# Optimization experiments

Hardware: AMD Instinct MI355X
Metric: run time of the kernel (lower is better)

## Reference

```python
import jax, jax.numpy as jnp
import numpy as np

N, E = 100000, 1600000
IN_C, HID, OUT_C = 128, 128, 64
HOPS, L = 2, 3
EPS = 1e-5


def setup_inputs() -> dict:
    key = jax.random.key(0)
    ks = jax.random.split(key, 16)
    x = jax.random.normal(ks[0], (N, IN_C), jnp.float32)
    edge_index = jax.random.randint(ks[1], (2, E), 0, N, dtype=jnp.int32).astype(jnp.int64)
    CAT = HID * (HOPS + 1)  # 384
    def lin(k, fan_in, fan_out, nstack):
        return jax.random.normal(k, (nstack, fan_in, fan_out), jnp.float32) / np.sqrt(fan_in)
    return {
        "x": x,
        "edge_index": edge_index,
        "W0": lin(ks[2], IN_C, HID, HOPS + 1),
        "b0": jnp.zeros((HOPS + 1, HID), jnp.float32),
        "W1": lin(ks[3], CAT, HID, HOPS + 1),
        "b1": jnp.zeros((HOPS + 1, HID), jnp.float32),
        "W2": lin(ks[4], CAT, OUT_C, HOPS + 1),
        "b2": jnp.zeros((HOPS + 1, OUT_C), jnp.float32),
        "bn0_g": jnp.ones((CAT,), jnp.float32),
        "bn0_b": jnp.zeros((CAT,), jnp.float32),
        "bn1_g": jnp.ones((CAT,), jnp.float32),
        "bn1_b": jnp.zeros((CAT,), jnp.float32),
        "fpW": jax.random.normal(ks[5], (OUT_C * (HOPS + 1), OUT_C), jnp.float32) / np.sqrt(OUT_C * (HOPS + 1)),
        "fpb": jnp.zeros((OUT_C,), jnp.float32),
    }


def reference(x, edge_index, W0, b0, W1, b1, W2, b2,
              bn0_g, bn0_b, bn1_g, bn1_b, fpW, fpb):
    row, col = edge_index[0], edge_index[1]
    # gcn_norm with add_self_loops=False, unit edge weights:
    # deg = scatter_add(1, col); w_e = deg^-1/2[row] * deg^-1/2[col]
    deg = jnp.zeros((N,), x.dtype).at[col].add(1.0)
    dinv = jnp.where(deg > 0, jax.lax.rsqrt(jnp.maximum(deg, 1.0)), 0.0)
    ew = dinv[row] * dinv[col]

    def spmm(h):
        # adj_t = SparseTensor(row=col, col=row, value=ew): out[col] += ew * h[row]
        return jax.ops.segment_sum(ew[:, None] * h[row], col, num_segments=N)

    def mixhop(h, W, b):
        outs = []
        for j in range(HOPS + 1):
            hj = h @ W[j] + b[j]          # lins[j](h)
            for _ in range(j):
                hj = spmm(hj)             # A^j applied j times
            outs.append(hj)
        return jnp.concatenate(outs, axis=1)

    def bn(h, g, bb):
        # BatchNorm1d in training mode: batch stats, biased variance
        mu = h.mean(axis=0)
        var = h.var(axis=0)
        return g * (h - mu) * jax.lax.rsqrt(var + EPS) + bb

    h = jax.nn.relu(bn(mixhop(x, W0, b0), bn0_g, bn0_b))   # dropout: identity (eval)
    h = jax.nn.relu(bn(mixhop(h, W1, b1), bn1_g, bn1_b))
    h = mixhop(h, W2, b2)
    return h @ fpW + fpb
```

## Files before the change

### kernel.cpp

```cpp
#include <hip/hip_runtime.h>
#include <cstdint>
#include <cstddef>

#define IN_C 128
#define HIDc 128
#define OUTc 64

using bf8 = __attribute__((ext_vector_type(8))) __bf16;
using f4  = __attribute__((ext_vector_type(4))) float;

__device__ __forceinline__ unsigned short f2bf(float f) {
    unsigned int u = __float_as_uint(f);
    unsigned int r = (u + 0x7FFFu + ((u >> 16) & 1u)) >> 16;
    return (unsigned short)r;
}
__device__ __forceinline__ float bf2f(unsigned short h) {
    return __uint_as_float(((unsigned int)h) << 16);
}

__global__ void k_detect(const long long* ei, int n_nodes, int* flag) {
    int t = threadIdx.x;
    long long v = ei[t];
    int ok = (v >= 0 && v < (long long)n_nodes) ? 1 : 0;
    unsigned long long m = __ballot(ok);
    if (t == 0) *flag = (m == ~0ull) ? 1 : 0;
}

__global__ void k_cvt_hist(const void* ei, int twoE, int E, const int* flag,
                           int* __restrict__ out, int* __restrict__ deg, int n) {
    int i = blockIdx.x * blockDim.x + threadIdx.x;
    if (i >= twoE) return;
    int v = (*flag) ? (int)((const long long*)ei)[i] : ((const int*)ei)[i];
    out[i] = v;
    if (i >= E && (unsigned)v < (unsigned)n) atomicAdd(&deg[v], 1);
}

__global__ void k_dinv(const int* __restrict__ deg, float* __restrict__ dinv, int n) {
    int i = blockIdx.x * blockDim.x + threadIdx.x;
    if (i < n) dinv[i] = (deg[i] > 0) ? rsqrtf((float)deg[i]) : 0.0f;
}

__global__ void k_alloc(const int* __restrict__ deg, int* __restrict__ base,
                        int* __restrict__ cursor, int* __restrict__ counter, int n) {
    int i = blockIdx.x * blockDim.x + threadIdx.x;
    int lane = threadIdx.x & 63;
    int val = (i < n) ? deg[i] : 0;
    int scan = val;
    #pragma unroll
    for (int off = 1; off < 64; off <<= 1) {
        int t = __shfl_up(scan, off);
        if (lane >= off) scan += t;
    }
    int excl = scan - val;
    int total = __shfl(scan, 63);
    int wb = 0;
    if (lane == 0) wb = atomicAdd(counter, total);
    wb = __shfl(wb, 0);
    if (i < n) { base[i] = wb + excl; cursor[i] = wb + excl; }
}

__global__ void k_scatter(const int* __restrict__ eint, int E,
                          const float* __restrict__ dinv, int n,
                          int* __restrict__ cursor, int2* __restrict__ ew) {
    int e = blockIdx.x * blockDim.x + threadIdx.x;
    if (e >= E) return;
    int r = eint[e];
    int c = eint[E + e];
    if ((unsigned)r >= (unsigned)n || (unsigned)c >= (unsigned)n) return;
    int p = atomicAdd(&cursor[c], 1);
    int2 v; v.x = r; v.y = __float_as_int(dinv[r] * dinv[c]);
    ew[p] = v;
}

__global__ void k_wprep(const float* __restrict__ W, unsigned short* __restrict__ Wt,
                        int K, int N) {
    int j = blockIdx.y;
    int idx = blockIdx.x * 256 + threadIdx.x;
    if (idx >= K * N) return;
    int k = idx / N, nn = idx - k * N;
    Wt[(size_t)j * N * K + (size_t)nn * K + k] = f2bf(W[(size_t)j * K * N + idx]);
}

__global__ void k_cast4(const float* __restrict__ x, unsigned short* __restrict__ y, int n4) {
    int i = blockIdx.x * 256 + threadIdx.x;
    if (i >= n4) return;
    float4 v = ((const float4*)x)[i];
    ushort4 o;
    o.x = f2bf(v.x); o.y = f2bf(v.y); o.z = f2bf(v.z); o.w = f2bf(v.w);
    ((ushort4*)y)[i] = o;
}

template<int PW, bool AFFINE>
__global__ __launch_bounds__(512) void k_mfma3(
    const unsigned short* __restrict__ A0, const unsigned short* __restrict__ A1,
    const unsigned short* __restrict__ A2, int W, int M, int K,
    const unsigned short* __restrict__ Bt, const float* __restrict__ bias,
    const float* __restrict__ scale, const float* __restrict__ shift,
    unsigned short* __restrict__ C0, unsigned short* __restrict__ C1,
    unsigned short* __restrict__ C2)
{
    constexpr int NT = 3 * PW;
    constexpr int TN = NT / 64;
    int t = threadIdx.x;
    int wave = t >> 6, lane = t & 63;
    int m16 = lane & 15, q = lane >> 4;
    int rowHalf = wave & 1, colQ = wave >> 1;
    int row0 = blockIdx.x * 128;

    size_t aoff[4];
    #pragma unroll
    for (int tm = 0; tm < 4; tm++) {
        int r = row0 + rowHalf * 64 + tm * 16 + m16;
        if (r >= M) r = M - 1;
        aoff[tm] = (size_t)r * W;
    }
    size_t boff[TN];
    #pragma unroll
    for (int tn = 0; tn < TN; tn++)
        boff[tn] = (size_t)(colQ * 16 * TN + tn * 16 + m16) * K;

    f4 acc[4][TN];
    #pragma unroll
    for (int i = 0; i < 4; i++)
        #pragma unroll
        for (int j = 0; j < TN; j++) acc[i][j] = (f4){0.f, 0.f, 0.f, 0.f};

    for (int kk = 0; kk < K; kk += 32) {
        int pi = kk / W;
        const unsigned short* Ap = (pi == 0) ? A0 : ((pi == 1) ? A1 : A2);
        int kl = kk - pi * W;

        uint4 a4[4];
        #pragma unroll
        for (int tm = 0; tm < 4; tm++)
            a4[tm] = *(const uint4*)&Ap[aoff[tm] + kl + q * 8];

        if (AFFINE) {
            int ch0 = kk + q * 8;
            float scv[8], shv[8];
            *(float4*)&scv[0] = *(const float4*)&scale[ch0];
            *(float4*)&scv[4] = *(const float4*)&scale[ch0 + 4];
            *(float4*)&shv[0] = *(const float4*)&shift[ch0];
            *(float4*)&shv[4] = *(const float4*)&shift[ch0 + 4];
            #pragma unroll
            for (int tm = 0; tm < 4; tm++) {
                unsigned int* w32 = (unsigned int*)&a4[tm];
                #pragma unroll
                for (int h = 0; h < 4; h++) {
                    unsigned int u = w32[h];
                    float lo = fmaxf(bf2f((unsigned short)(u & 0xffff)) * scv[2*h]     + shv[2*h],     0.f);
                    float hi = fmaxf(bf2f((unsigned short)(u >> 16))    * scv[2*h + 1] + shv[2*h + 1], 0.f);
                    w32[h] = (unsigned int)f2bf(lo) | ((unsigned int)f2bf(hi) << 16);
                }
            }
        }

        bf8 bfr[TN];
        #pragma unroll
        for (int tn = 0; tn < TN; tn++)
            bfr[tn] = *(const bf8*)&Bt[boff[tn] + kk + q * 8];

        #pragma unroll
        for (int tm = 0; tm < 4; tm++) {
            bf8 af = *(const bf8*)&a4[tm];
            #pragma unroll
            for (int tn = 0; tn < TN; tn++)
                acc[tm][tn] = __builtin_amdgcn_mfma_f32_16x16x32_bf16(
                    af, bfr[tn], acc[tm][tn], 0, 0, 0);
        }
    }

    #pragma unroll
    for (int tn = 0; tn < TN; tn++) {
        int col_base = colQ * 16 * TN + tn * 16;
        int j  = col_base / PW;
        int cc = col_base - j * PW + m16;
        unsigned short* Cj = (j == 0) ? C0 : ((j == 1) ? C1 : C2);
        float bi = bias[col_base + m16];
        #pragma unroll
        for (int tm = 0; tm < 4; tm++) {
            #pragma unroll
            for (int r = 0; r < 4; r++) {
                int row = row0 + rowHalf * 64 + tm * 16 + q * 4 + r;
                if (row >= M) continue;
                Cj[(size_t)row * PW + cc] = f2bf(acc[tm][tn][r] + bi);
            }
        }
    }
}

__global__ __launch_bounds__(256) void k_mfma_fin(
    const unsigned short* __restrict__ A0, const unsigned short* __restrict__ A1,
    const unsigned short* __restrict__ A2, int W, int M, int K,
    const unsigned short* __restrict__ Bt, const float* __restrict__ bias,
    float* __restrict__ C, int ldc)
{
    constexpr int TM = 2, TN = 4;
    int t = threadIdx.x;
    int wave = t >> 6, lane = t & 63;
    int m16 = lane & 15, q = lane >> 4;
    int row0 = blockIdx.x * 128;
    int wr = wave * 32;

    size_t aoff[TM];
    #pragma unroll
    for (int tm = 0; tm < TM; tm++) {
        int r = row0 + wr + tm * 16 + m16;
        if (r >= M) r = M - 1;
        aoff[tm] = (size_t)r * W;
    }
    size_t boff[TN];
    #pragma unroll
    for (int tn = 0; tn < TN; tn++)
        boff[tn] = (size_t)(tn * 16 + m16) * K;

    f4 acc[TM][TN];
    #pragma unroll
    for (int i = 0; i < TM; i++)
        #pragma unroll
        for (int j = 0; j < TN; j++) acc[i][j] = (f4){0.f, 0.f, 0.f, 0.f};

    for (int kk = 0; kk < K; kk += 32) {
        int pi = kk / W;
        const unsigned short* Ap = (pi == 0) ? A0 : ((pi == 1) ? A1 : A2);
        int kl = kk - pi * W;

        bf8 af[TM], bfr[TN];
        #pragma unroll
        for (int tm = 0; tm < TM; tm++)
            af[tm] = *(const bf8*)&Ap[aoff[tm] + kl + q * 8];
        #pragma unroll
        for (int tn = 0; tn < TN; tn++)
            bfr[tn] = *(const bf8*)&Bt[boff[tn] + kk + q * 8];
        #pragma unroll
        for (int tm = 0; tm < TM; tm++)
            #pragma unroll
            for (int tn = 0; tn < TN; tn++)
                acc[tm][tn] = __builtin_amdgcn_mfma_f32_16x16x32_bf16(
                    af[tm], bfr[tn], acc[tm][tn], 0, 0, 0);
    }

    #pragma unroll
    for (int tm = 0; tm < TM; tm++) {
        #pragma unroll
        for (int tn = 0; tn < TN; tn++) {
            int col = tn * 16 + m16;
            float bi = bias[col];
            #pragma unroll
            for (int r = 0; r < 4; r++) {
                int row = row0 + wr + tm * 16 + q * 4 + r;
                if (row >= M) continue;
                C[(size_t)row * ldc + col] = acc[tm][tn][r] + bi;
            }
        }
    }
}

template<int V, bool DUAL>
__global__ __launch_bounds__(256) void k_spmm(
    const unsigned short* __restrict__ S1, const unsigned short* __restrict__ S2,
    unsigned short* __restrict__ D1, unsigned short* __restrict__ D2, int width,
    const int* __restrict__ base, const int* __restrict__ deg,
    const int2* __restrict__ ew, int n)
{
    int node = blockIdx.x * 4 + threadIdx.y;
    if (node >= n) return;
    int tx = threadIdx.x;
    float a1[V], a2[V];
    #pragma unroll
    for (int v = 0; v < V; v++) { a1[v] = 0.f; if (DUAL) a2[v] = 0.f; }
    int b = base[node], end = b + deg[node];
    const unsigned short* P1 = S1 + tx * V;
    const unsigned short* P2 = DUAL ? (S2 + tx * V) : nullptr;
    constexpr int UN = 8;
    int e = b;
    for (; e + UN <= end; e += UN) {
        int2 ev[UN];
        #pragma unroll
        for (int u = 0; u < UN; u++) ev[u] = ew[e + u];
        unsigned int g1[UN], g2[UN];
        #pragma unroll
        for (int u = 0; u < UN; u++) {
            if (V == 2) g1[u] = *(const unsigned int*)(P1 + (size_t)ev[u].x * width);
            else        g1[u] = P1[(size_t)ev[u].x * width];
            if (DUAL) {
                if (V == 2) g2[u] = *(const unsigned int*)(P2 + (size_t)ev[u].x * width);
                else        g2[u] = P2[(size_t)ev[u].x * width];
            }
        }
        #pragma unroll
        for (int u = 0; u < UN; u++) {
            float we = __int_as_float(ev[u].y);
            if (V == 2) {
                a1[0] += we * bf2f((unsigned short)(g1[u] & 0xffff));
                a1[1] += we * bf2f((unsigned short)(g1[u] >> 16));
                if (DUAL) {
                    a2[0] += we * bf2f((unsigned short)(g2[u] & 0xffff));
                    a2[1] += we * bf2f((unsigned short)(g2[u] >> 16));
                }
            } else {
                a1[0] += we * bf2f((unsigned short)g1[u]);
                if (DUAL) a2[0] += we * bf2f((unsigned short)g2[u]);
            }
        }
    }
    for (; e < end; ++e) {
        int2 ev = ew[e];
        float we = __int_as_float(ev.y);
        if (V == 2) {
            unsigned int u1 = *(const unsigned int*)(P1 + (size_t)ev.x * width);
            a1[0] += we * bf2f((unsigned short)(u1 & 0xffff));
            a1[1] += we * bf2f((unsigned short)(u1 >> 16));
            if (DUAL) {
                unsigned int u2 = *(const unsigned int*)(P2 + (size_t)ev.x * width);
                a2[0] += we * bf2f((unsigned short)(u2 & 0xffff));
                a2[1] += we * bf2f((unsigned short)(u2 >> 16));
            }
        } else {
            a1[0] += we * bf2f(P1[(size_t)ev.x * width]);
            if (DUAL) a2[0] += we * bf2f(P2[(size_t)ev.x * width]);
        }
    }
    size_t o = (size_t)node * width + tx * V;
    if (V == 2) {
        ushort2 o1; o1.x = f2bf(a1[0]); o1.y = f2bf(a1[1]);
        *(ushort2*)&D1[o] = o1;
        if (DUAL) { ushort2 o2; o2.x = f2bf(a2[0]); o2.y = f2bf(a2[1]);
                    *(ushort2*)&D2[o] = o2; }
    } else {
        D1[o] = f2bf(a1[0]);
        if (DUAL) D2[o] = f2bf(a2[0]);
    }
}

__global__ void k_bnstats(const unsigned short* __restrict__ p0,
                          const unsigned short* __restrict__ p1,
                          const unsigned short* __restrict__ p2,
                          float* __restrict__ sums, float* __restrict__ sumsq, int n)
{
    int c = threadIdx.x;
    int cc = c & 127;
    int pi = c >> 7;
    const unsigned short* src = (pi == 0) ? p0 : ((pi == 1) ? p1 : p2);
    float s = 0.f, s2 = 0.f;
    for (int r = blockIdx.x; r < n; r += gridDim.x) {
        float v = bf2f(src[(size_t)r * 128 + cc]);
        s += v; s2 += v * v;
    }
    atomicAdd(&sums[c], s);
    atomicAdd(&sumsq[c], s2);
}

__global__ void k_bnfin(const float* __restrict__ sums, const float* __restrict__ sumsq,
                        const float* __restrict__ g, const float* __restrict__ bb,
                        float* __restrict__ scale, float* __restrict__ shift,
                        int cat, float invn)
{
    int c = threadIdx.x;
    if (c >= cat) return;
    float mu  = sums[c] * invn;
    float var = sumsq[c] * invn - mu * mu;
    float sc  = g[c] * rsqrtf(var + 1e-5f);
    scale[c] = sc;
    shift[c] = bb[c] - mu * sc;
}

__global__ void k_diag(float* out, float val, int n) {
    int i = blockIdx.x * blockDim.x + threadIdx.x;
    if (i < n) out[i] = val;
}

extern "C" void kernel_launch(void* const* d_in, const int* in_sizes, int n_in,
                              void* d_out, int out_size, void* d_ws, size_t ws_size,
                              hipStream_t stream)
{
    const float* x    = (const float*)d_in[0];
    const void*  ei   = d_in[1];
    const float* W0   = (const float*)d_in[2];
    const float* b0   = (const float*)d_in[3];
    const float* W1   = (const float*)d_in[4];
    const float* b1   = (const float*)d_in[5];
    const float* W2   = (const float*)d_in[6];
    const float* b2   = (const float*)d_in[7];
    const float* bn0g = (const float*)d_in[8];
    const float* bn0b = (const float*)d_in[9];
    const float* bn1g = (const float*)d_in[10];
    const float* bn1b = (const float*)d_in[11];
    const float* fpW  = (const float*)d_in[12];
    const float* fpb  = (const float*)d_in[13];
    float* out = (float*)d_out;

    const int N    = in_sizes[0] / IN_C;
    const int twoE = in_sizes[1];
    const int E    = twoE / 2;

    char* p = (char*)d_ws;
    auto alloc = [&](size_t bytes) -> char* {
        char* r = p; p += (bytes + 255) & ~(size_t)255; return r;
    };
    unsigned short* U[6];
    for (int i = 0; i < 6; i++) U[i] = (unsigned short*)alloc((size_t)N * 128 * 2);
    unsigned short* Wt0 = (unsigned short*)alloc((size_t)3 * 128 * 128 * 2);
    unsigned short* Wt1 = (unsigned short*)alloc((size_t)3 * 384 * 128 * 2);
    unsigned short* Wt2 = (unsigned short*)alloc((size_t)3 * 384 * 64 * 2);
    unsigned short* WtF = (unsigned short*)alloc((size_t)192 * 64 * 2);
    float* dinv  = (float*)alloc((size_t)N * 4);
    int2*  ew    = (int2*)alloc((size_t)E * 8);
    float* sums  = (float*)alloc(2 * 384 * 4);
    float* sumsq = sums + 384;
    float* scale = (float*)alloc(384 * 4);
    float* shift = (float*)alloc(384 * 4);
    int* deg     = (int*)alloc((size_t)N * 4);
    int* base    = (int*)alloc((size_t)N * 4);
    int* cursor  = (int*)alloc((size_t)N * 4);
    int* eint    = (int*)alloc((size_t)twoE * 4);
    int* counter = (int*)alloc(4);
    int* flag    = (int*)alloc(4);

    size_t required = (size_t)(p - (char*)d_ws);
    if (required > ws_size) {
        k_diag<<<(out_size + 255) / 256, 256, 0, stream>>>(
            out, (float)(ws_size >> 20), out_size);
        return;
    }

    const int T = 256;
    dim3 spmm_blk(64, 4);
    int  spmm_grid = (N + 3) / 4;
    int  gx128 = (N + 127) / 128;

    k_wprep<<<dim3((128 * 128 + 255) / 256, 3), T, 0, stream>>>(W0, Wt0, 128, 128);
    k_wprep<<<dim3((384 * 128 + 255) / 256, 3), T, 0, stream>>>(W1, Wt1, 384, 128);
    k_wprep<<<dim3((384 * 64  + 255) / 256, 3), T, 0, stream>>>(W2, Wt2, 384, 64);
    k_wprep<<<dim3((192 * 64  + 255) / 256, 1), T, 0, stream>>>(fpW, WtF, 192, 64);
    unsigned short* Xb = U[3];
    k_cast4<<<((N * 128 / 4) + 255) / 256, T, 0, stream>>>(x, Xb, N * 128 / 4);

    hipMemsetAsync(deg, 0, (size_t)N * 4, stream);
    hipMemsetAsync(counter, 0, 4, stream);
    k_detect<<<1, 64, 0, stream>>>((const long long*)ei, N, flag);
    k_cvt_hist<<<(twoE + T - 1) / T, T, 0, stream>>>(ei, twoE, E, flag, eint, deg, N);
    k_dinv<<<(N + T - 1) / T, T, 0, stream>>>(deg, dinv, N);
    k_alloc<<<(N + T - 1) / T, T, 0, stream>>>(deg, base, cursor, counter, N);
    k_scatter<<<(E + T - 1) / T, T, 0, stream>>>(eint, E, dinv, N, cursor, ew);

    k_mfma3<128, false><<<gx128, 512, 0, stream>>>(Xb, Xb, Xb, 128, N, 128,
        Wt0, b0, nullptr, nullptr, U[0], U[1], U[2]);
    k_spmm<2, true ><<<spmm_grid, spmm_blk, 0, stream>>>(U[1], U[2], U[4], U[5], 128,
                                                         base, deg, ew, N);
    k_spmm<2, false><<<spmm_grid, spmm_blk, 0, stream>>>(U[5], nullptr, U[3], nullptr, 128,
                                                         base, deg, ew, N);
    hipMemsetAsync(sums, 0, 2 * 384 * 4, stream);
    k_bnstats<<<2048, 384, 0, stream>>>(U[0], U[4], U[3], sums, sumsq, N);
    k_bnfin<<<1, 384, 0, stream>>>(sums, sumsq, bn0g, bn0b, scale, shift, 384, 1.0f / N);

    k_mfma3<128, true><<<gx128, 512, 0, stream>>>(U[0], U[4], U[3], 128, N, 384,
        Wt1, b1, scale, shift, U[1], U[2], U[5]);
    k_spmm<2, true ><<<spmm_grid, spmm_blk, 0, stream>>>(U[2], U[5], U[0], U[4], 128,
                                                         base, deg, ew, N);
    k_spmm<2, false><<<spmm_grid, spmm_blk, 0, stream>>>(U[4], nullptr, U[3], nullptr, 128,
                                                         base, deg, ew, N);
    hipMemsetAsync(sums, 0, 2 * 384 * 4, stream);
    k_bnstats<<<2048, 384, 0, stream>>>(U[1], U[0], U[3], sums, sumsq, N);
    k_bnfin<<<1, 384, 0, stream>>>(sums, sumsq, bn1g, bn1b, scale, shift, 384, 1.0f / N);

    unsigned short* V2a = U[2];
    unsigned short* V2b = U[2] + (size_t)N * 64;
    unsigned short* V4a = U[4];
    unsigned short* V4b = U[4] + (size_t)N * 64;
    unsigned short* V5a = U[5];
    unsigned short* V5b = U[5] + (size_t)N * 64;
    k_mfma3<64, true><<<gx128, 512, 0, stream>>>(U[1], U[0], U[3], 128, N, 384,
        Wt2, b2, scale, shift, V2a, V2b, V4a);
    k_spmm<1, true ><<<spmm_grid, spmm_blk, 0, stream>>>(V2b, V4a, V4b, V5a, 64,
                                                         base, deg, ew, N);
    k_spmm<1, false><<<spmm_grid, spmm_blk, 0, stream>>>(V5a, nullptr, V5b, nullptr, 64,
                                                         base, deg, ew, N);

    k_mfma_fin<<<gx128, T, 0, stream>>>(V2a, V4b, V5b, 64, N, 192, WtF, fpb, out, 64);
}
```

Before: 1.381 ms.

## Split GEMMs per output block, prefetch operands, apply BN+ReLU in separate pass

Replaces the 512-thread fused three-way GEMM with a 256-thread kernel that computes one output block per grid-y index, and adds register double-buffering of the A/B fragments for the next k-step. The BatchNorm affine and ReLU, previously recomputed inside the GEMM A-load for every column tile, move into a standalone in-place elementwise kernel over the 384 concatenated channels. This gives smaller per-block tiles and more blocks, and overlaps loads with MFMA. In exchange the A matrix is now re-read once per output block, and BN application costs an extra full read/write pass over the activations.

New measurement: 1.502 ms. +8.8%, slower.

```diff
diff --git a/kernel.cpp b/kernel.cpp
--- a/kernel.cpp
+++ b/kernel.cpp
@@ -90,117 +90,24 @@
     ((ushort4*)y)[i] = o;
 }
 
-template<int PW, bool AFFINE>
-__global__ __launch_bounds__(512) void k_mfma3(
+template<int PW, bool BFOUT>
+__global__ __launch_bounds__(256) void k_gemm(
     const unsigned short* __restrict__ A0, const unsigned short* __restrict__ A1,
     const unsigned short* __restrict__ A2, int W, int M, int K,
-    const unsigned short* __restrict__ Bt, const float* __restrict__ bias,
-    const float* __restrict__ scale, const float* __restrict__ shift,
+    const unsigned short* __restrict__ Bt,
+    const float* __restrict__ bias,
     unsigned short* __restrict__ C0, unsigned short* __restrict__ C1,
-    unsigned short* __restrict__ C2)
-{
-    constexpr int NT = 3 * PW;
-    constexpr int TN = NT / 64;
+    unsigned short* __restrict__ C2, float* __restrict__ Cf)
+{
+    constexpr int TM = (PW == 128) ? 4 : 2;
+    constexpr int TN = 4;
     int t = threadIdx.x;
     int wave = t >> 6, lane = t & 63;
     int m16 = lane & 15, q = lane >> 4;
-    int rowHalf = wave & 1, colQ = wave >> 1;
+    int j = blockIdx.y;
     int row0 = blockIdx.x * 128;
-
-    size_t aoff[4];
-    #pragma unroll
-    for (int tm = 0; tm < 4; tm++) {
-        int r = row0 + rowHalf * 64 + tm * 16 + m16;
-        if (r >= M) r = M - 1;
-        aoff[tm] = (size_t)r * W;
-    }
-    size_t boff[TN];
-    #pragma unroll
-    for (int tn = 0; tn < TN; tn++)
-        boff[tn] = (size_t)(colQ * 16 * TN + tn * 16 + m16) * K;
-
-    f4 acc[4][TN];
-    #pragma unroll
-    for (int i = 0; i < 4; i++)
-        #pragma unroll
-        for (int j = 0; j < TN; j++) acc[i][j] = (f4){0.f, 0.f, 0.f, 0.f};
-
-    for (int kk = 0; kk < K; kk += 32) {
-        int pi = kk / W;
-        const unsigned short* Ap = (pi == 0) ? A0 : ((pi == 1) ? A1 : A2);
-        int kl = kk - pi * W;
-
-        uint4 a4[4];
-        #pragma unroll
-        for (int tm = 0; tm < 4; tm++)
-            a4[tm] = *(const uint4*)&Ap[aoff[tm] + kl + q * 8];
-
-        if (AFFINE) {
-            int ch0 = kk + q * 8;
-            float scv[8], shv[8];
-            *(float4*)&scv[0] = *(const float4*)&scale[ch0];
-            *(float4*)&scv[4] = *(const float4*)&scale[ch0 + 4];
-            *(float4*)&shv[0] = *(const float4*)&shift[ch0];
-            *(float4*)&shv[4] = *(const float4*)&shift[ch0 + 4];
-            #pragma unroll
-            for (int tm = 0; tm < 4; tm++) {
-                unsigned int* w32 = (unsigned int*)&a4[tm];
-                #pragma unroll
-                for (int h = 0; h < 4; h++) {
-                    unsigned int u = w32[h];
-                    float lo = fmaxf(bf2f((unsigned short)(u & 0xffff)) * scv[2*h]     + shv[2*h],     0.f);
-                    float hi = fmaxf(bf2f((unsigned short)(u >> 16))    * scv[2*h + 1] + shv[2*h + 1], 0.f);
-                    w32[h] = (unsigned int)f2bf(lo) | ((unsigned int)f2bf(hi) << 16);
-                }
-            }
-        }
-
-        bf8 bfr[TN];
-        #pragma unroll
-        for (int tn = 0; tn < TN; tn++)
-            bfr[tn] = *(const bf8*)&Bt[boff[tn] + kk + q * 8];
-
-        #pragma unroll
-        for (int tm = 0; tm < 4; tm++) {
-            bf8 af = *(const bf8*)&a4[tm];
-            #pragma unroll
-            for (int tn = 0; tn < TN; tn++)
-                acc[tm][tn] = __builtin_amdgcn_mfma_f32_16x16x32_bf16(
-                    af, bfr[tn], acc[tm][tn], 0, 0, 0);
-        }
-    }
-
-    #pragma unroll
-    for (int tn = 0; tn < TN; tn++) {
-        int col_base = colQ * 16 * TN + tn * 16;
-        int j  = col_base / PW;
-        int cc = col_base - j * PW + m16;
-        unsigned short* Cj = (j == 0) ? C0 : ((j == 1) ? C1 : C2);
-        float bi = bias[col_base + m16];
-        #pragma unroll
-        for (int tm = 0; tm < 4; tm++) {
-            #pragma unroll
-            for (int r = 0; r < 4; r++) {
-                int row = row0 + rowHalf * 64 + tm * 16 + q * 4 + r;
-                if (row >= M) continue;
-                Cj[(size_t)row * PW + cc] = f2bf(acc[tm][tn][r] + bi);
-            }
-        }
-    }
-}
-
-__global__ __launch_bounds__(256) void k_mfma_fin(
-    const unsigned short* __restrict__ A0, const unsigned short* __restrict__ A1,
-    const unsigned short* __restrict__ A2, int W, int M, int K,
-    const unsigned short* __restrict__ Bt, const float* __restrict__ bias,
-    float* __restrict__ C, int ldc)
-{
-    constexpr int TM = 2, TN = 4;
-    int t = threadIdx.x;
-    int wave = t >> 6, lane = t & 63;
-    int m16 = lane & 15, q = lane >> 4;
-    int row0 = blockIdx.x * 128;
-    int wr = wave * 32;
+    int wr = (PW == 128) ? (wave & 1) * 64 : wave * 32;
+    int wc = (PW == 128) ? (wave >> 1) * 64 : 0;
 
     size_t aoff[TM];
     #pragma unroll
@@ -212,45 +119,59 @@
     size_t boff[TN];
     #pragma unroll
     for (int tn = 0; tn < TN; tn++)
-        boff[tn] = (size_t)(tn * 16 + m16) * K;
+        boff[tn] = (size_t)(j * PW + wc + tn * 16 + m16) * K;
 
     f4 acc[TM][TN];
     #pragma unroll
     for (int i = 0; i < TM; i++)
         #pragma unroll
-        for (int j = 0; j < TN; j++) acc[i][j] = (f4){0.f, 0.f, 0.f, 0.f};
-
-    for (int kk = 0; kk < K; kk += 32) {
+        for (int jj = 0; jj < TN; jj++) acc[i][jj] = (f4){0.f, 0.f, 0.f, 0.f};
+
+    auto loadA = [&](int kk, bf8* dst) {
         int pi = kk / W;
         const unsigned short* Ap = (pi == 0) ? A0 : ((pi == 1) ? A1 : A2);
         int kl = kk - pi * W;
-
-        bf8 af[TM], bfr[TN];
         #pragma unroll
         for (int tm = 0; tm < TM; tm++)
-            af[tm] = *(const bf8*)&Ap[aoff[tm] + kl + q * 8];
+            dst[tm] = *(const bf8*)&Ap[aoff[tm] + kl + q * 8];
+    };
+    auto loadB = [&](int kk, bf8* dst) {
         #pragma unroll
         for (int tn = 0; tn < TN; tn++)
-            bfr[tn] = *(const bf8*)&Bt[boff[tn] + kk + q * 8];
+            dst[tn] = *(const bf8*)&Bt[boff[tn] + kk + q * 8];
+    };
+
+    bf8 aC[TM], bC[TN], aN[TM], bN[TN];
+    loadA(0, aC); loadB(0, bC);
+    for (int kk = 0; kk < K; kk += 32) {
+        int kn = kk + 32;
+        if (kn < K) { loadA(kn, aN); loadB(kn, bN); }
         #pragma unroll
         for (int tm = 0; tm < TM; tm++)
             #pragma unroll
             for (int tn = 0; tn < TN; tn++)
                 acc[tm][tn] = __builtin_amdgcn_mfma_f32_16x16x32_bf16(
-                    af[tm], bfr[tn], acc[tm][tn], 0, 0, 0);
-    }
-
+                    aC[tm], bC[tn], acc[tm][tn], 0, 0, 0);
+        #pragma unroll
+        for (int tm = 0; tm < TM; tm++) aC[tm] = aN[tm];
+        #pragma unroll
+        for (int tn = 0; tn < TN; tn++) bC[tn] = bN[tn];
+    }
+
+    unsigned short* Cj = (j == 0) ? C0 : ((j == 1) ? C1 : C2);
     #pragma unroll
     for (int tm = 0; tm < TM; tm++) {
         #pragma unroll
         for (int tn = 0; tn < TN; tn++) {
-            int col = tn * 16 + m16;
-            float bi = bias[col];
+            int col = wc + tn * 16 + m16;
+            float bi = bias[j * PW + col];
             #pragma unroll
             for (int r = 0; r < 4; r++) {
                 int row = row0 + wr + tm * 16 + q * 4 + r;
                 if (row >= M) continue;
-                C[(size_t)row * ldc + col] = acc[tm][tn][r] + bi;
+                float v = acc[tm][tn][r] + bi;
+                if (BFOUT) Cj[(size_t)row * PW + col] = f2bf(v);
+                else       Cf[(size_t)row * PW + col] = v;
             }
         }
     }
@@ -363,6 +284,23 @@
     float sc  = g[c] * rsqrtf(var + 1e-5f);
     scale[c] = sc;
     shift[c] = bb[c] - mu * sc;
+}
+
+__global__ void k_bnapply(unsigned short* __restrict__ p0, unsigned short* __restrict__ p1,
+                          unsigned short* __restrict__ p2,
+                          const float* __restrict__ scale, const float* __restrict__ shift,
+                          int n)
+{
+    int c = threadIdx.x;
+    int cc = c & 127;
+    int pi = c >> 7;
+    unsigned short* src = (pi == 0) ? p0 : ((pi == 1) ? p1 : p2);
+    float sc = scale[c], sh = shift[c];
+    for (int r = blockIdx.x; r < n; r += gridDim.x) {
+        size_t idx = (size_t)r * 128 + cc;
+        float v = bf2f(src[idx]) * sc + sh;
+        src[idx] = f2bf(fmaxf(v, 0.0f));
+    }
 }
 
 __global__ void k_diag(float* out, float val, int n) {
@@ -444,8 +382,8 @@
     k_alloc<<<(N + T - 1) / T, T, 0, stream>>>(deg, base, cursor, counter, N);
     k_scatter<<<(E + T - 1) / T, T, 0, stream>>>(eint, E, dinv, N, cursor, ew);
 
-    k_mfma3<128, false><<<gx128, 512, 0, stream>>>(Xb, Xb, Xb, 128, N, 128,
-        Wt0, b0, nullptr, nullptr, U[0], U[1], U[2]);
+    k_gemm<128, true><<<dim3(gx128, 3), T, 0, stream>>>(Xb, Xb, Xb, 128, N, 128,
+        Wt0, b0, U[0], U[1], U[2], nullptr);
     k_spmm<2, true ><<<spmm_grid, spmm_blk, 0, stream>>>(U[1], U[2], U[4], U[5], 128,
                                                          base, deg, ew, N);
     k_spmm<2, false><<<spmm_grid, spmm_blk, 0, stream>>>(U[5], nullptr, U[3], nullptr, 128,
@@ -453,9 +391,10 @@
     hipMemsetAsync(sums, 0, 2 * 384 * 4, stream);
     k_bnstats<<<2048, 384, 0, stream>>>(U[0], U[4], U[3], sums, sumsq, N);
     k_bnfin<<<1, 384, 0, stream>>>(sums, sumsq, bn0g, bn0b, scale, shift, 384, 1.0f / N);
-
-    k_mfma3<128, true><<<gx128, 512, 0, stream>>>(U[0], U[4], U[3], 128, N, 384,
-        Wt1, b1, scale, shift, U[1], U[2], U[5]);
+    k_bnapply<<<2048, 384, 0, stream>>>(U[0], U[4], U[3], scale, shift, N);
+
+    k_gemm<128, true><<<dim3(gx128, 3), T, 0, stream>>>(U[0], U[4], U[3], 128, N, 384,
+        Wt1, b1, U[1], U[2], U[5], nullptr);
     k_spmm<2, true ><<<spmm_grid, spmm_blk, 0, stream>>>(U[2], U[5], U[0], U[4], 128,
                                                          base, deg, ew, N);
     k_spmm<2, false><<<spmm_grid, spmm_blk, 0, stream>>>(U[4], nullptr, U[3], nullptr, 128,
@@ -463,6 +402,7 @@
     hipMemsetAsync(sums, 0, 2 * 384 * 4, stream);
     k_bnstats<<<2048, 384, 0, stream>>>(U[1], U[0], U[3], sums, sumsq, N);
     k_bnfin<<<1, 384, 0, stream>>>(sums, sumsq, bn1g, bn1b, scale, shift, 384, 1.0f / N);
+    k_bnapply<<<2048, 384, 0, stream>>>(U[1], U[0], U[3], scale, shift, N);
 
     unsigned short* V2a = U[2];
     unsigned short* V2b = U[2] + (size_t)N * 64;
@@ -470,12 +410,13 @@
     unsigned short* V4b = U[4] + (size_t)N * 64;
     unsigned short* V5a = U[5];
     unsigned short* V5b = U[5] + (size_t)N * 64;
-    k_mfma3<64, true><<<gx128, 512, 0, stream>>>(U[1], U[0], U[3], 128, N, 384,
-        Wt2, b2, scale, shift, V2a, V2b, V4a);
+    k_gemm<64, true><<<dim3(gx128, 3), T, 0, stream>>>(U[1], U[0], U[3], 128, N, 384,
+        Wt2, b2, V2a, V2b, V4a, nullptr);
     k_spmm<1, true ><<<spmm_grid, spmm_blk, 0, stream>>>(V2b, V4a, V4b, V5a, 64,
                                                          base, deg, ew, N);
     k_spmm<1, false><<<spmm_grid, spmm_blk, 0, stream>>>(V5a, nullptr, V5b, nullptr, 64,
                                                          base, deg, ew, N);
 
-    k_mfma_fin<<<gx128, T, 0, stream>>>(V2a, V4b, V5b, 64, N, 192, WtF, fpb, out, 64);
-}
+    k_gemm<64, false><<<dim3(gx128, 1), T, 0, stream>>>(V2a, V4b, V5b, 64, N, 192,
+        WtF, fpb, nullptr, nullptr, nullptr, out);
+}
```
